# Kernel tuning notes

Hardware: AMD Instinct MI355X
Metric: run time of the kernel (lower is better)

Reference implementation:

```python
import jax, jax.numpy as jnp
import numpy as np

EMBED_DIM = 1024


def setup_inputs() -> dict:
    key = jax.random.key(0)
    ks = jax.random.split(key, 7)
    B, S, D = 4, 2048, EMBED_DIM
    scale = 1.0 / np.sqrt(D)
    x = jax.random.normal(ks[0], (B, S, D), dtype=jnp.float32)
    # nn.Linear weights stored as [out, in]; we keep [in, out] for x @ W
    Wq = jax.random.normal(ks[1], (D, D), dtype=jnp.float32) * scale
    bq = jax.random.normal(ks[2], (D,), dtype=jnp.float32) * scale
    Wk = jax.random.normal(ks[3], (D, D), dtype=jnp.float32) * scale
    bk = jax.random.normal(ks[4], (D,), dtype=jnp.float32) * scale
    Wv = jax.random.normal(ks[5], (D, D), dtype=jnp.float32) * scale
    bv = jax.random.normal(ks[6], (D,), dtype=jnp.float32) * scale
    return {"x": x, "Wq": Wq, "bq": bq, "Wk": Wk, "bk": bk, "Wv": Wv, "bv": bv}


def reference(x, Wq, bq, Wk, bk, Wv, bv):
    # Single-head attention (num_heads unused in original module).
    q = x @ Wq + bq            # [B, S, D]
    k = x @ Wk + bk            # [B, S, D]
    v = x @ Wv + bv            # [B, S, D]
    inv_sqrt_d = 1.0 / jnp.sqrt(jnp.asarray(x.shape[-1], x.dtype))
    scores = jnp.einsum("bsd,btd->bst", q, k) * inv_sqrt_d  # [B, S, S]
    attn = jax.nn.softmax(scores, axis=-1)
    return jnp.einsum("bst,btd->bsd", attn, v)
```

## Files before the change

kernel.cpp:

```cpp
#include <hip/hip_runtime.h>
#include <hip/hip_bf16.h>


using floatx4 = __attribute__((ext_vector_type(4))) float;
using shortx8 = __attribute__((ext_vector_type(8))) short;
using shortx4 = __attribute__((ext_vector_type(4))) short;

__device__ __forceinline__ short f2bf(float f) {
    __hip_bfloat16 h = __float2bfloat16(f);
    return *reinterpret_cast<short*>(&h);
}
__device__ __forceinline__ float bf2f(short s) {
    unsigned u = (unsigned)(unsigned short)s << 16;
    return __uint_as_float(u);
}

#define MFMA16(a, b, c) __builtin_amdgcn_mfma_f32_16x16x32_bf16((a), (b), (c), 0, 0, 0)

__device__ __forceinline__ void gld_lds16(const void* g, void* l) {
    __builtin_amdgcn_global_load_lds(
        (const __attribute__((address_space(1))) void*)g,
        (__attribute__((address_space(3))) void*)l, 16, 0, 0);
}

template<int MH>
__device__ __forceinline__ void rdA(const short* sAb, int wm, int lrow,
                                    int xo0, int xo1, shortx8 (&af)[4][2]) {
    const short* base = sAb + ((wm << 7) + (MH << 6) + lrow) * 64;
#pragma unroll
    for (int i = 0; i < 4; ++i) {
        af[i][0] = *reinterpret_cast<const shortx8*>(base + i * 1024 + xo0);
        af[i][1] = *reinterpret_cast<const shortx8*>(base + i * 1024 + xo1);
    }
}
template<int NH>
__device__ __forceinline__ void rdB(const short* sBb, int wn, int lrow,
                                    int xo0, int xo1, shortx8 (&bf)[4][2]) {
    const short* base = sBb + ((wn << 6) + (NH << 5) + lrow) * 64;
#pragma unroll
    for (int j = 0; j < 2; ++j) {
        bf[NH * 2 + j][0] = *reinterpret_cast<const shortx8*>(base + j * 1024 + xo0);
        bf[NH * 2 + j][1] = *reinterpret_cast<const shortx8*>(base + j * 1024 + xo1);
    }
}
template<int MH, int NH>
__device__ __forceinline__ void mfq(shortx8 (&af)[4][2], shortx8 (&bf)[4][2],
                                    floatx4 (&acc)[8][4]) {
    __builtin_amdgcn_s_setprio(1);
#pragma unroll
    for (int i = 0; i < 4; ++i) {
#pragma unroll
        for (int j = 0; j < 2; ++j) {
            acc[MH * 4 + i][NH * 2 + j] =
                MFMA16(af[i][0], bf[NH * 2 + j][0], acc[MH * 4 + i][NH * 2 + j]);
            acc[MH * 4 + i][NH * 2 + j] =
                MFMA16(af[i][1], bf[NH * 2 + j][1], acc[MH * 4 + i][NH * 2 + j]);
        }
    }
    __builtin_amdgcn_s_setprio(0);
}

__device__ __forceinline__ void gemm256_loop8(
    const short* __restrict__ A, const short* __restrict__ B,
    int lda, int ldb, int K,
    short* sA, short* sB, floatx4 (&acc)[8][4], int t)
{
    const int w = t >> 6, l = t & 63;
    const int wm = w >> 2, wn = w & 3;
    const int lrow = l & 15, quad = l >> 4, r8 = lrow & 7;
    const int xo0 = (quad ^ r8) << 3;
    const int xo1 = ((quad + 4) ^ r8) << 3;
    const int rr = t >> 3;
    const int gsw = ((t & 7) ^ (rr & 7)) << 3;
    const short* gA0 = A + (size_t)rr * lda + gsw;
    const short* gA1 = A + (size_t)(128 + rr) * lda + gsw;
    const short* gB0 = B + (size_t)rr * ldb + gsw;
    const short* gB1 = B + (size_t)(128 + rr) * ldb + gsw;
    const int wofs = w << 9;

    auto stage = [&](const short* g, int ld, int kt, short* ldsb) {
        const short* p = g + kt;
        gld_lds16(p, ldsb + wofs);
        gld_lds16(p + (size_t)(ld << 6), ldsb + wofs + 4096);
    };

    shortx8 af[4][2], bf[4][2];
    const int NT = K >> 6;

    stage(gA0, lda, 0, sA);
    stage(gA1, lda, 0, sA + 8192);
    stage(gB0, ldb, 0, sB);
    stage(gB1, ldb, 0, sB + 8192);
    stage(gB0, ldb, 64, sB + 16384);
    stage(gB1, ldb, 64, sB + 16384 + 8192);
    asm volatile("s_waitcnt vmcnt(4)" ::: "memory");
    __builtin_amdgcn_s_barrier();

    for (int T = 0; T < NT; T += 2) {
        const bool more = (T + 2) < NT;
        const int ktA1 = (T + 1) << 6;
        const int ktN2 = (T + 2) << 6;
        const int ktB3 = (T + 3) << 6;
        short* sA0 = sA;           short* sB0 = sB;
        short* sA1 = sA + 16384;   short* sB1 = sB + 16384;

        rdA<0>(sA0, wm, lrow, xo0, xo1, af);
        rdB<0>(sB0, wn, lrow, xo0, xo1, bf);
        stage(gA0, lda, ktA1, sA1);
        asm volatile("s_waitcnt lgkmcnt(8)" ::: "memory");
        __builtin_amdgcn_s_barrier();
        asm volatile("s_waitcnt lgkmcnt(0)" ::: "memory");
        __builtin_amdgcn_sched_barrier(0);
        mfq<0, 0>(af, bf, acc);
        __builtin_amdgcn_s_barrier();

        rdB<1>(sB0, wn, lrow, xo0, xo1, bf);
        stage(gA1, lda, ktA1, sA1 + 8192);
        __builtin_amdgcn_s_barrier();
        asm volatile("s_waitcnt lgkmcnt(0)" ::: "memory");
        __builtin_amdgcn_sched_barrier(0);
        mfq<0, 1>(af, bf, acc);
        __builtin_amdgcn_s_barrier();

        rdA<1>(sA0, wm, lrow, xo0, xo1, af);
        if (more) stage(gB0, ldb, ktN2, sB0);
        __builtin_amdgcn_s_barrier();
        asm volatile("s_waitcnt lgkmcnt(0)" ::: "memory");
        __builtin_amdgcn_sched_barrier(0);
        mfq<1, 0>(af, bf, acc);
        __builtin_amdgcn_s_barrier();

        if (more) stage(gB1, ldb, ktN2, sB0 + 8192);
        __builtin_amdgcn_s_barrier();
        __builtin_amdgcn_sched_barrier(0);
        mfq<1, 1>(af, bf, acc);
        if (more) { asm volatile("s_waitcnt vmcnt(4)" ::: "memory"); }
        else      { asm volatile("s_waitcnt vmcnt(0)" ::: "memory"); }
        __builtin_amdgcn_s_barrier();

        rdA<0>(sA1, wm, lrow, xo0, xo1, af);
        rdB<0>(sB1, wn, lrow, xo0, xo1, bf);
        if (more) stage(gA0, lda, ktN2, sA0);
        asm volatile("s_waitcnt lgkmcnt(8)" ::: "memory");
        __builtin_amdgcn_s_barrier();
        asm volatile("s_waitcnt lgkmcnt(0)" ::: "memory");
        __builtin_amdgcn_sched_barrier(0);
        mfq<0, 0>(af, bf, acc);
        __builtin_amdgcn_s_barrier();

        rdB<1>(sB1, wn, lrow, xo0, xo1, bf);
        if (more) stage(gA1, lda, ktN2, sA0 + 8192);
        __builtin_amdgcn_s_barrier();
        asm volatile("s_waitcnt lgkmcnt(0)" ::: "memory");
        __builtin_amdgcn_sched_barrier(0);
        mfq<0, 1>(af, bf, acc);
        __builtin_amdgcn_s_barrier();

        rdA<1>(sA1, wm, lrow, xo0, xo1, af);
        if (more) stage(gB0, ldb, ktB3, sB1);
        __builtin_amdgcn_s_barrier();
        asm volatile("s_waitcnt lgkmcnt(0)" ::: "memory");
        __builtin_amdgcn_sched_barrier(0);
        mfq<1, 0>(af, bf, acc);
        __builtin_amdgcn_s_barrier();

        if (more) stage(gB1, ldb, ktB3, sB1 + 8192);
        __builtin_amdgcn_s_barrier();
        __builtin_amdgcn_sched_barrier(0);
        mfq<1, 1>(af, bf, acc);
        if (more) { asm volatile("s_waitcnt vmcnt(4)" ::: "memory"); }
        __builtin_amdgcn_s_barrier();
    }
}

__device__ __forceinline__ void rdB2(const short* sBb, int wn, int lrow,
                                     int xo0, int xo1, shortx8 (&bf)[2][2]) {
    const short* base = sBb + ((wn << 5) + lrow) * 64;
#pragma unroll
    for (int j = 0; j < 2; ++j) {
        bf[j][0] = *reinterpret_cast<const shortx8*>(base + j * 1024 + xo0);
        bf[j][1] = *reinterpret_cast<const shortx8*>(base + j * 1024 + xo1);
    }
}
template<int MH>
__device__ __forceinline__ void mfqA(shortx8 (&af)[4][2], shortx8 (&bf)[2][2],
                                     floatx4 (&acc)[8][2]) {
    __builtin_amdgcn_s_setprio(1);
#pragma unroll
    for (int i = 0; i < 4; ++i) {
#pragma unroll
        for (int j = 0; j < 2; ++j) {
            acc[MH * 4 + i][j] = MFMA16(af[i][0], bf[j][0], acc[MH * 4 + i][j]);
            acc[MH * 4 + i][j] = MFMA16(af[i][1], bf[j][1], acc[MH * 4 + i][j]);
        }
    }
    __builtin_amdgcn_s_setprio(0);
}

__device__ __forceinline__ void gemm256x128_loop(
    const short* __restrict__ A, const short* __restrict__ B,
    int lda, int ldb, int K,
    short* sA, short* sB, floatx4 (&acc)[8][2], int t)
{
    const int w = t >> 6, l = t & 63;
    const int wm = w >> 2, wn = w & 3;
    const int lrow = l & 15, quad = l >> 4, r8 = lrow & 7;
    const int xo0 = (quad ^ r8) << 3;
    const int xo1 = ((quad + 4) ^ r8) << 3;
    const int rr = t >> 3;
    const int gsw = ((t & 7) ^ (rr & 7)) << 3;
    const short* gA0 = A + (size_t)rr * lda + gsw;
    const short* gA1 = A + (size_t)(128 + rr) * lda + gsw;
    const short* gB0 = B + (size_t)rr * ldb + gsw;
    const int wofs = w << 9;

    auto stage = [&](const short* g, int ld, int kt, short* ldsb) {
        const short* p = g + kt;
        gld_lds16(p, ldsb + wofs);
        gld_lds16(p + (size_t)(ld << 6), ldsb + wofs + 4096);
    };

    shortx8 af[4][2], bf[2][2];
    const int NT = K >> 6;
    short* sA0 = sA;           short* sB0 = sB;
    short* sA1 = sA + 16384;   short* sB1 = sB + 8192;

    stage(gA0, lda, 0, sA0); stage(gA1, lda, 0, sA0 + 8192);
    stage(gB0, ldb, 0, sB0);
    stage(gA0, lda, 64, sA1); stage(gA1, lda, 64, sA1 + 8192);
    stage(gB0, ldb, 64, sB1);
    asm volatile("s_waitcnt vmcnt(6)" ::: "memory");
    __builtin_amdgcn_s_barrier();

    for (int T = 0; T < NT; T += 2) {
        const bool m2 = (T + 2) < NT;
        const int ktA1 = (T + 1) << 6;
        const int kt2  = (T + 2) << 6;
        const int kt3  = (T + 3) << 6;

        rdA<0>(sA0, wm, lrow, xo0, xo1, af);
        rdB2(sB0, wn, lrow, xo0, xo1, bf);
        if (T > 0) { stage(gA0, lda, ktA1, sA1); stage(gA1, lda, ktA1, sA1 + 8192); }
        asm volatile("s_waitcnt lgkmcnt(8)" ::: "memory");
        __builtin_amdgcn_s_barrier();
        asm volatile("s_waitcnt lgkmcnt(0)" ::: "memory");
        __builtin_amdgcn_sched_barrier(0);
        mfqA<0>(af, bf, acc);
        __builtin_amdgcn_s_barrier();

        rdA<1>(sA0, wm, lrow, xo0, xo1, af);
        if (m2) stage(gB0, ldb, kt2, sB0);
        __builtin_amdgcn_s_barrier();
        asm volatile("s_waitcnt lgkmcnt(0)" ::: "memory");
        __builtin_amdgcn_sched_barrier(0);
        mfqA<1>(af, bf, acc);
        if (m2) { asm volatile("s_waitcnt vmcnt(2)" ::: "memory"); }
        else    { asm volatile("s_waitcnt vmcnt(0)" ::: "memory"); }
        __builtin_amdgcn_s_barrier();

        rdA<0>(sA1, wm, lrow, xo0, xo1, af);
        rdB2(sB1, wn, lrow, xo0, xo1, bf);
        if (m2) { stage(gA0, lda, kt2, sA0); stage(gA1, lda, kt2, sA0 + 8192); }
        asm volatile("s_waitcnt lgkmcnt(8)" ::: "memory");
        __builtin_amdgcn_s_barrier();
        asm volatile("s_waitcnt lgkmcnt(0)" ::: "memory");
        __builtin_amdgcn_sched_barrier(0);
        mfqA<0>(af, bf, acc);
        __builtin_amdgcn_s_barrier();

        rdA<1>(sA1, wm, lrow, xo0, xo1, af);
        if (m2) stage(gB0, ldb, kt3, sB1);
        __builtin_amdgcn_s_barrier();
        asm volatile("s_waitcnt lgkmcnt(0)" ::: "memory");
        __builtin_amdgcn_sched_barrier(0);
        mfqA<1>(af, bf, acc);
        if (m2) { asm volatile("s_waitcnt vmcnt(2)" ::: "memory"); }
        __builtin_amdgcn_s_barrier();
    }
}

__device__ __forceinline__ void gemm_loop(
    const short* __restrict__ A, const short* __restrict__ B,
    size_t lda, size_t ldb, int K,
    short* as_, short* bs_, floatx4 (&acc)[4][4], int w, int l)
{
    const int lr8 = l >> 3;
    const int swz = ((l & 7) ^ lr8) * 8;
    const int lrow = l & 15, quad = l >> 4;
    const int wr = w >> 1, wc = w & 1;
    const int r8r = lrow & 7;
    const short* pa = A + (size_t)(w * 32 + lr8) * lda + swz;
    const short* pb = B + (size_t)(w * 32 + lr8) * ldb + swz;
    short* la = as_ + w * 4 * 512;
    short* lb = bs_ + w * 4 * 512;

    for (int kt = 0; kt < K; kt += 64) {
        for (int c = 0; c < 4; ++c) {
            gld_lds16(pa + (size_t)c * 8 * lda + kt, la + c * 512);
            gld_lds16(pb + (size_t)c * 8 * ldb + kt, lb + c * 512);
        }
        __syncthreads();
        for (int kk = 0; kk < 64; kk += 32) {
            const int xoff = (((kk >> 3) + quad) ^ r8r) << 3;
            shortx8 af[4], bfr[4];
            for (int i = 0; i < 4; ++i)
                af[i] = *reinterpret_cast<const shortx8*>(
                    &as_[(size_t)(wr * 64 + i * 16 + lrow) * 64 + xoff]);
            for (int j = 0; j < 4; ++j)
                bfr[j] = *reinterpret_cast<const shortx8*>(
                    &bs_[(size_t)(wc * 64 + j * 16 + lrow) * 64 + xoff]);
            for (int i = 0; i < 4; ++i)
                for (int j = 0; j < 4; ++j)
                    acc[i][j] = MFMA16(af[i], bfr[j], acc[i][j]);
        }
        __syncthreads();
    }
}

__global__ __launch_bounds__(256) void prep_kernel(
    const float* __restrict__ X,
    const float* __restrict__ Wq, const float* __restrict__ Wk,
    const float* __restrict__ Wv,
    const float* __restrict__ bq, const float* __restrict__ bk,
    const float* __restrict__ bv,
    short* __restrict__ Xb, short* __restrict__ Wt,
    float* __restrict__ bcat)
{
    const int id = blockIdx.x, t = threadIdx.x;
    if (id < 4096) {
        size_t i = ((size_t)id * 256 + t) * 8;
        float4 v0 = *reinterpret_cast<const float4*>(X + i);
        float4 v1 = *reinterpret_cast<const float4*>(X + i + 4);
        shortx8 s;
        s[0] = f2bf(v0.x); s[1] = f2bf(v0.y); s[2] = f2bf(v0.z); s[3] = f2bf(v0.w);
        s[4] = f2bf(v1.x); s[5] = f2bf(v1.y); s[6] = f2bf(v1.z); s[7] = f2bf(v1.w);
        *reinterpret_cast<shortx8*>(Xb + i) = s;
    } else if (id < 4864) {
        __shared__ float tl[64][65];
        const int wid = id - 4096;
        const int z = wid >> 8, t16 = wid & 255;
        const float* src = (z == 0) ? Wq : (z == 1) ? Wk : Wv;
        short* dst = Wt + (size_t)z * 1024 * 1024;
        const int k0 = (t16 >> 4) * 64, n0 = (t16 & 15) * 64;
        for (int i = t; i < 64 * 64; i += 256) {
            int r = i >> 6, c = i & 63;
            tl[r][c] = src[(size_t)(k0 + r) * 1024 + n0 + c];
        }
        __syncthreads();
        for (int i = t; i < 64 * 64; i += 256) {
            int r = i >> 6, c = i & 63;
            dst[(size_t)(n0 + r) * 1024 + k0 + c] = f2bf(tl[c][r]);
        }
    } else {
        const int z = id - 4864;
        const float* bsrc = (z == 0) ? bq : (z == 1) ? bk : bv;
        for (int i = t; i < 1024; i += 256) bcat[z * 1024 + i] = bsrc[i];
    }
}

__global__ __launch_bounds__(512, 2) void qkv_qk_kernel(
    const short* __restrict__ Xb, const short* __restrict__ Wt,
    const float* __restrict__ bcat, short* __restrict__ dQ,
    short* __restrict__ dK)
{
    __shared__ short sA[2 * 16384];
    __shared__ short sB[2 * 16384];
    const int t = threadIdx.x;
    const int m0 = blockIdx.x * 256, n0 = blockIdx.y * 256;
    const int w = t >> 6, l = t & 63;
    const int wm = w >> 2, wn = w & 3, lrow = l & 15, quad = l >> 4;
    const int sec = n0 >> 10;

    floatx4 acc[8][4];
#pragma unroll
    for (int i = 0; i < 8; ++i)
#pragma unroll
        for (int j = 0; j < 4; ++j) acc[i][j] = floatx4{0.f, 0.f, 0.f, 0.f};

    gemm256_loop8(Xb + (size_t)m0 * 1024, Wt + (size_t)n0 * 1024,
                  1024, 1024, 1024, sA, sB, acc, t);

    short* outN = (sec == 0) ? dQ : dK;
#pragma unroll
    for (int i = 0; i < 8; ++i) {
        int rbase = m0 + wm * 128 + i * 16 + quad * 4;
#pragma unroll
        for (int j = 0; j < 4; ++j) {
            int coln = n0 + wn * 64 + j * 16 + lrow;
            int col = coln & 1023;
            float bvv = bcat[coln];
#pragma unroll
            for (int r = 0; r < 4; ++r)
                outN[(size_t)(rbase + r) * 1024 + col] =
                    f2bf(acc[i][j][r] + bvv);
        }
    }
}

__global__ __launch_bounds__(256) void qkv_v_kernel(
    const short* __restrict__ Xb, const short* __restrict__ Wt,
    const float* __restrict__ bcat, short* __restrict__ Vt)
{
    __shared__ short as_[128 * 64];
    __shared__ short bs_[128 * 64];
    const int t = threadIdx.x, w = t >> 6, l = t & 63;
    const int m0 = blockIdx.x * 128;
    const int n0 = 2048 + blockIdx.y * 128;
    const int wr = w >> 1, wc = w & 1, lrow = l & 15, quad = l >> 4;

    floatx4 acc[4][4];
    for (int i = 0; i < 4; ++i)
        for (int j = 0; j < 4; ++j) acc[i][j] = floatx4{0.f, 0.f, 0.f, 0.f};

    gemm_loop(Xb + (size_t)m0 * 1024, Wt + (size_t)n0 * 1024,
              1024, 1024, 1024, as_, bs_, acc, w, l);

    for (int i = 0; i < 4; ++i) {
        int rbase = m0 + wr * 64 + i * 16 + quad * 4;
        int b = rbase >> 11, sl = rbase & 2047;
        for (int j = 0; j < 4; ++j) {
            int coln = n0 + wc * 64 + j * 16 + lrow;
            int col = coln & 1023;
            float bvv = bcat[coln];
            shortx4 s;
            for (int r = 0; r < 4; ++r) s[r] = f2bf(acc[i][j][r] + bvv);
            *reinterpret_cast<shortx4*>(
                &Vt[((size_t)b * 1024 + col) * 2048 + sl]) = s;
        }
    }
}

__global__ __launch_bounds__(512, 2) void scores_kernel(
    const short* __restrict__ dQ, const short* __restrict__ dK,
    short* __restrict__ P, float* __restrict__ partials, int row_start)
{
    __shared__ short sA[2 * 16384];
    __shared__ short sB[2 * 16384];
    const int t = threadIdx.x;
    int bx = blockIdx.x, by = blockIdx.y;
    if (gridDim.x == 32) {
        const int c = bx & 7;
        const int k = (bx >> 3) + (by << 2);
        const int bb = c >> 1, half = c & 1;
        bx = bb * 8 + (k & 3) + 4 * half;
        by = k >> 2;
    }
    const int m0 = bx * 256;
    const int n0 = by * 256;
    const int g0 = row_start + m0;
    const int b = g0 >> 11;
    const int w = t >> 6, l = t & 63;
    const int wm = w >> 2, wn = w & 3, lrow = l & 15, quad = l >> 4;

    floatx4 acc[8][4];
#pragma unroll
    for (int i = 0; i < 8; ++i)
#pragma unroll
        for (int j = 0; j < 4; ++j) acc[i][j] = floatx4{0.f, 0.f, 0.f, 0.f};

    gemm256_loop8(dQ + (size_t)g0 * 1024, dK + ((size_t)b * 2048 + n0) * 1024,
                  1024, 1024, 1024, sA, sB, acc, t);

    float* sred = reinterpret_cast<float*>(sA);
#pragma unroll
    for (int i = 0; i < 8; ++i) {
        int rl = wm * 128 + i * 16 + quad * 4;
        int rloc = m0 + rl;
        float rs[4] = {0.f, 0.f, 0.f, 0.f};
#pragma unroll
        for (int j = 0; j < 4; ++j) {
            int col = n0 + wn * 64 + j * 16 + lrow;
#pragma unroll
            for (int r = 0; r < 4; ++r) {
                short pb = f2bf(__expf(acc[i][j][r] * 0.03125f - 20.0f));
                P[(size_t)(rloc + r) * 2048 + col] = pb;
                rs[r] += bf2f(pb);
            }
        }
#pragma unroll
        for (int r = 0; r < 4; ++r)
            for (int m = 1; m <= 8; m <<= 1)
                rs[r] += __shfl_xor(rs[r], m, 64);
        if (lrow == 0)
#pragma unroll
            for (int r = 0; r < 4; ++r)
                sred[(rl + r) * 4 + wn] = rs[r];
    }
    __syncthreads();
    if (t < 256) {
        float s = sred[t * 4] + sred[t * 4 + 1] + sred[t * 4 + 2] + sred[t * 4 + 3];
        partials[(size_t)(row_start + m0 + t) * 8 + by] = s;
    }
}

__global__ __launch_bounds__(512, 2) void pv_kernel(
    const short* __restrict__ P, const short* __restrict__ Vt,
    const float* __restrict__ partials, float* __restrict__ Out, int row_start)
{
    __shared__ short sA[2 * 16384];
    __shared__ short sB[2 * 8192];
    const int t = threadIdx.x;
    int bx = blockIdx.x, by = blockIdx.y;
    if (gridDim.x == 32) {
        const int c = bx & 7;
        const int k = (bx >> 3) + (by << 2);
        const int bb = c >> 1, half = c & 1;
        bx = bb * 8 + (k & 3) + 4 * half;
        by = k >> 2;
    }
    const int m0 = bx * 256;
    const int n0 = by * 128;
    const int g0 = row_start + m0;
    const int b = g0 >> 11;
    const int w = t >> 6, l = t & 63;
    const int wm = w >> 2, wn = w & 3, lrow = l & 15, quad = l >> 4;

    floatx4 acc[8][2];
#pragma unroll
    for (int i = 0; i < 8; ++i)
#pragma unroll
        for (int j = 0; j < 2; ++j) acc[i][j] = floatx4{0.f, 0.f, 0.f, 0.f};

    gemm256x128_loop(P + (size_t)m0 * 2048, Vt + ((size_t)b * 1024 + n0) * 2048,
                     2048, 2048, 2048, sA, sB, acc, t);

#pragma unroll
    for (int ii = 0; ii < 8; ++ii) {
        int rl = wm * 128 + (ii >> 2) * 64 + (ii & 3) * 16 + quad * 4;
        int rglb = row_start + m0 + rl;
        float is[4];
#pragma unroll
        for (int r = 0; r < 4; ++r) {
            const float4* pp =
                reinterpret_cast<const float4*>(&partials[(size_t)(rglb + r) * 8]);
            float4 p0 = pp[0], p1 = pp[1];
            float s = (p0.x + p0.y) + (p0.z + p0.w) +
                      (p1.x + p1.y) + (p1.z + p1.w);
            is[r] = 1.0f / s;
        }
#pragma unroll
        for (int j = 0; j < 2; ++j) {
            int col = n0 + wn * 32 + j * 16 + lrow;
#pragma unroll
            for (int r = 0; r < 4; ++r)
                Out[(size_t)(rglb + r) * 1024 + col] = acc[ii][j][r] * is[r];
        }
    }
}

extern "C" void kernel_launch(void* const* d_in, const int* in_sizes, int n_in,
                              void* d_out, int out_size, void* d_ws, size_t ws_size,
                              hipStream_t stream)
{
    const float* x  = (const float*)d_in[0];
    const float* Wq = (const float*)d_in[1];
    const float* bq = (const float*)d_in[2];
    const float* Wk = (const float*)d_in[3];
    const float* bk = (const float*)d_in[4];
    const float* Wv = (const float*)d_in[5];
    const float* bv = (const float*)d_in[6];
    float* out = (float*)d_out;

    short* dQ = (short*)d_out;
    short* dK = dQ + (size_t)8192 * 1024;

    char* ws = (char*)d_ws;
    short* Wt   = (short*)ws;
    float* bcat = (float*)(ws + 6291456);
    float* partials = (float*)(ws + 6291456 + 12288);
    short* Vt   = (short*)(ws + 6291456 + 12288 + 262144);
    char*  region = ws + 6291456 + 12288 + 262144 + 16777216;
    const size_t base = 6291456 + 12288 + 262144 + 16777216;

    size_t avail = ws_size > base ? ws_size - base : 0;
    long rows_fit = (long)(avail / 4096);
    int chunk = (int)(rows_fit & ~255L);
    if (chunk > 8192) chunk = 8192;
    if (chunk < 256) chunk = 256;
    short* Xb = (short*)region;
    short* P  = (short*)region;

    prep_kernel<<<dim3(4867), 256, 0, stream>>>(x, Wq, Wk, Wv, bq, bk, bv,
                                                Xb, Wt, bcat);
    qkv_qk_kernel<<<dim3(32, 8), 512, 0, stream>>>(Xb, Wt, bcat, dQ, dK);
    qkv_v_kernel<<<dim3(64, 8), 256, 0, stream>>>(Xb, Wt, bcat, Vt);

    for (int rs = 0; rs < 8192; rs += chunk) {
        int rows = 8192 - rs;
        if (rows > chunk) rows = chunk;
        scores_kernel<<<dim3(rows / 256, 8), 512, 0, stream>>>(dQ, dK, P, partials, rs);
        pv_kernel<<<dim3(rows / 256, 8), 512, 0, stream>>>(P, Vt, partials, out, rs);
    }
}
```

Before: 233.7 us.

## Merge QK and V projection kernels; shrink PV tiles to 128x128

The Q/K projection and the V projection are combined into one launch. V blocks now use 256x128 tiles with 512 threads in place of a separate 128x128 kernel, which removes a kernel boundary and the tail idle time between the two launches. The PV kernel, in exchange, moves from 256x128 tiles with 512 threads to 128x128 tiles with 256 threads, and its block swizzle is adjusted for the doubled grid. This gives PV more blocks for occupancy but less operand reuse per block.

```diff
diff --git a/kernel.cpp b/kernel.cpp
--- a/kernel.cpp
+++ b/kernel.cpp
@@ -358,74 +358,73 @@
     }
 }
 
-__global__ __launch_bounds__(512, 2) void qkv_qk_kernel(
+__global__ __launch_bounds__(512, 2) void qkv_all_kernel(
     const short* __restrict__ Xb, const short* __restrict__ Wt,
     const float* __restrict__ bcat, short* __restrict__ dQ,
-    short* __restrict__ dK)
+    short* __restrict__ dK, short* __restrict__ Vt)
 {
     __shared__ short sA[2 * 16384];
     __shared__ short sB[2 * 16384];
     const int t = threadIdx.x;
-    const int m0 = blockIdx.x * 256, n0 = blockIdx.y * 256;
     const int w = t >> 6, l = t & 63;
     const int wm = w >> 2, wn = w & 3, lrow = l & 15, quad = l >> 4;
-    const int sec = n0 >> 10;
-
-    floatx4 acc[8][4];
-#pragma unroll
-    for (int i = 0; i < 8; ++i)
-#pragma unroll
-        for (int j = 0; j < 4; ++j) acc[i][j] = floatx4{0.f, 0.f, 0.f, 0.f};
-
-    gemm256_loop8(Xb + (size_t)m0 * 1024, Wt + (size_t)n0 * 1024,
-                  1024, 1024, 1024, sA, sB, acc, t);
-
-    short* outN = (sec == 0) ? dQ : dK;
-#pragma unroll
-    for (int i = 0; i < 8; ++i) {
-        int rbase = m0 + wm * 128 + i * 16 + quad * 4;
-#pragma unroll
-        for (int j = 0; j < 4; ++j) {
-            int coln = n0 + wn * 64 + j * 16 + lrow;
-            int col = coln & 1023;
-            float bvv = bcat[coln];
-#pragma unroll
-            for (int r = 0; r < 4; ++r)
-                outN[(size_t)(rbase + r) * 1024 + col] =
-                    f2bf(acc[i][j][r] + bvv);
-        }
-    }
-}
-
-__global__ __launch_bounds__(256) void qkv_v_kernel(
-    const short* __restrict__ Xb, const short* __restrict__ Wt,
-    const float* __restrict__ bcat, short* __restrict__ Vt)
-{
-    __shared__ short as_[128 * 64];
-    __shared__ short bs_[128 * 64];
-    const int t = threadIdx.x, w = t >> 6, l = t & 63;
-    const int m0 = blockIdx.x * 128;
-    const int n0 = 2048 + blockIdx.y * 128;
-    const int wr = w >> 1, wc = w & 1, lrow = l & 15, quad = l >> 4;
-
-    floatx4 acc[4][4];
-    for (int i = 0; i < 4; ++i)
-        for (int j = 0; j < 4; ++j) acc[i][j] = floatx4{0.f, 0.f, 0.f, 0.f};
-
-    gemm_loop(Xb + (size_t)m0 * 1024, Wt + (size_t)n0 * 1024,
-              1024, 1024, 1024, as_, bs_, acc, w, l);
-
-    for (int i = 0; i < 4; ++i) {
-        int rbase = m0 + wr * 64 + i * 16 + quad * 4;
-        int b = rbase >> 11, sl = rbase & 2047;
-        for (int j = 0; j < 4; ++j) {
-            int coln = n0 + wc * 64 + j * 16 + lrow;
-            int col = coln & 1023;
-            float bvv = bcat[coln];
-            shortx4 s;
-            for (int r = 0; r < 4; ++r) s[r] = f2bf(acc[i][j][r] + bvv);
-            *reinterpret_cast<shortx4*>(
-                &Vt[((size_t)b * 1024 + col) * 2048 + sl]) = s;
+    const int m0 = blockIdx.x * 256;
+
+    if (blockIdx.y < 8) {
+        const int n0 = blockIdx.y * 256;
+        const int sec = n0 >> 10;
+
+        floatx4 acc[8][4];
+#pragma unroll
+        for (int i = 0; i < 8; ++i)
+#pragma unroll
+            for (int j = 0; j < 4; ++j) acc[i][j] = floatx4{0.f, 0.f, 0.f, 0.f};
+
+        gemm256_loop8(Xb + (size_t)m0 * 1024, Wt + (size_t)n0 * 1024,
+                      1024, 1024, 1024, sA, sB, acc, t);
+
+        short* outN = (sec == 0) ? dQ : dK;
+#pragma unroll
+        for (int i = 0; i < 8; ++i) {
+            int rbase = m0 + wm * 128 + i * 16 + quad * 4;
+#pragma unroll
+            for (int j = 0; j < 4; ++j) {
+                int coln = n0 + wn * 64 + j * 16 + lrow;
+                int col = coln & 1023;
+                float bvv = bcat[coln];
+#pragma unroll
+                for (int r = 0; r < 4; ++r)
+                    outN[(size_t)(rbase + r) * 1024 + col] =
+                        f2bf(acc[i][j][r] + bvv);
+            }
+        }
+    } else {
+        const int n0 = 2048 + (blockIdx.y - 8) * 128;
+
+        floatx4 acc[8][2];
+#pragma unroll
+        for (int i = 0; i < 8; ++i)
+#pragma unroll
+            for (int j = 0; j < 2; ++j) acc[i][j] = floatx4{0.f, 0.f, 0.f, 0.f};
+
+        gemm256x128_loop(Xb + (size_t)m0 * 1024, Wt + (size_t)n0 * 1024,
+                         1024, 1024, 1024, sA, sB, acc, t);
+
+#pragma unroll
+        for (int ii = 0; ii < 8; ++ii) {
+            int rbase = m0 + wm * 128 + (ii >> 2) * 64 + (ii & 3) * 16 + quad * 4;
+            int b = rbase >> 11, sl = rbase & 2047;
+#pragma unroll
+            for (int j = 0; j < 2; ++j) {
+                int coln = n0 + wn * 32 + j * 16 + lrow;
+                int col = coln & 1023;
+                float bvv = bcat[coln];
+                shortx4 s;
+#pragma unroll
+                for (int r = 0; r < 4; ++r) s[r] = f2bf(acc[ii][j][r] + bvv);
+                *reinterpret_cast<shortx4*>(
+                    &Vt[((size_t)b * 1024 + col) * 2048 + sl]) = s;
+            }
         }
     }
 }
@@ -493,43 +492,38 @@
     }
 }
 
-__global__ __launch_bounds__(512, 2) void pv_kernel(
+__global__ __launch_bounds__(256) void pv_kernel(
     const short* __restrict__ P, const short* __restrict__ Vt,
     const float* __restrict__ partials, float* __restrict__ Out, int row_start)
 {
-    __shared__ short sA[2 * 16384];
-    __shared__ short sB[2 * 8192];
-    const int t = threadIdx.x;
+    __shared__ short as_[128 * 64];
+    __shared__ short bs_[128 * 64];
+    const int t = threadIdx.x, w = t >> 6, l = t & 63;
     int bx = blockIdx.x, by = blockIdx.y;
-    if (gridDim.x == 32) {
+    if (gridDim.x == 64) {
         const int c = bx & 7;
-        const int k = (bx >> 3) + (by << 2);
+        const int k = (bx >> 3) + (by << 3);
         const int bb = c >> 1, half = c & 1;
-        bx = bb * 8 + (k & 3) + 4 * half;
-        by = k >> 2;
-    }
-    const int m0 = bx * 256;
+        bx = bb * 16 + (k & 7) + 8 * half;
+        by = k >> 3;
+    }
+    const int m0 = bx * 128;
     const int n0 = by * 128;
     const int g0 = row_start + m0;
     const int b = g0 >> 11;
-    const int w = t >> 6, l = t & 63;
-    const int wm = w >> 2, wn = w & 3, lrow = l & 15, quad = l >> 4;
-
-    floatx4 acc[8][2];
-#pragma unroll
-    for (int i = 0; i < 8; ++i)
-#pragma unroll
-        for (int j = 0; j < 2; ++j) acc[i][j] = floatx4{0.f, 0.f, 0.f, 0.f};
-
-    gemm256x128_loop(P + (size_t)m0 * 2048, Vt + ((size_t)b * 1024 + n0) * 2048,
-                     2048, 2048, 2048, sA, sB, acc, t);
-
-#pragma unroll
-    for (int ii = 0; ii < 8; ++ii) {
-        int rl = wm * 128 + (ii >> 2) * 64 + (ii & 3) * 16 + quad * 4;
-        int rglb = row_start + m0 + rl;
+    const int wr = w >> 1, wc = w & 1, lrow = l & 15, quad = l >> 4;
+
+    floatx4 acc[4][4];
+    for (int i = 0; i < 4; ++i)
+        for (int j = 0; j < 4; ++j) acc[i][j] = floatx4{0.f, 0.f, 0.f, 0.f};
+
+    gemm_loop(P + (size_t)m0 * 2048, Vt + ((size_t)b * 1024 + n0) * 2048,
+              2048, 2048, 2048, as_, bs_, acc, w, l);
+
+    for (int i = 0; i < 4; ++i) {
+        int rloc = m0 + wr * 64 + i * 16 + quad * 4;
+        int rglb = row_start + rloc;
         float is[4];
-#pragma unroll
         for (int r = 0; r < 4; ++r) {
             const float4* pp =
                 reinterpret_cast<const float4*>(&partials[(size_t)(rglb + r) * 8]);
@@ -538,12 +532,10 @@
                       (p1.x + p1.y) + (p1.z + p1.w);
             is[r] = 1.0f / s;
         }
-#pragma unroll
-        for (int j = 0; j < 2; ++j) {
-            int col = n0 + wn * 32 + j * 16 + lrow;
-#pragma unroll
+        for (int j = 0; j < 4; ++j) {
+            int col = n0 + wc * 64 + j * 16 + lrow;
             for (int r = 0; r < 4; ++r)
-                Out[(size_t)(rglb + r) * 1024 + col] = acc[ii][j][r] * is[r];
+                Out[(size_t)(rglb + r) * 1024 + col] = acc[i][j][r] * is[r];
         }
     }
 }
@@ -582,13 +574,12 @@
 
     prep_kernel<<<dim3(4867), 256, 0, stream>>>(x, Wq, Wk, Wv, bq, bk, bv,
                                                 Xb, Wt, bcat);
-    qkv_qk_kernel<<<dim3(32, 8), 512, 0, stream>>>(Xb, Wt, bcat, dQ, dK);
-    qkv_v_kernel<<<dim3(64, 8), 256, 0, stream>>>(Xb, Wt, bcat, Vt);
+    qkv_all_kernel<<<dim3(32, 16), 512, 0, stream>>>(Xb, Wt, bcat, dQ, dK, Vt);
 
     for (int rs = 0; rs < 8192; rs += chunk) {
         int rows = 8192 - rs;
         if (rows > chunk) rows = chunk;
         scores_kernel<<<dim3(rows / 256, 8), 512, 0, stream>>>(dQ, dK, P, partials, rs);
-        pv_kernel<<<dim3(rows / 256, 8), 512, 0, stream>>>(P, Vt, partials, out, rs);
-    }
-}
+        pv_kernel<<<dim3(rows / 128, 8), 256, 0, stream>>>(P, Vt, partials, out, rs);
+    }
+}
```

New measurement: 232.2 us. No clear change (-0.6%).
